# Optimization experiments

Hardware: AMD Instinct MI355X
Metric: run time of the kernel (lower is better)

## Reference

```python
import jax, jax.numpy as jnp
import numpy as np
from math import sqrt

B = 128        # graphs
P = 256        # nodes per graph
N = B * P      # total nodes
E = 524288     # edges (avg degree 16)
S = 32         # seed queries per graph
DQ = DK = DV = 128
H = 4          # heads


def setup_inputs() -> dict:
    key = jax.random.key(0)
    ks = jax.random.split(key, 10)
    Q = jax.random.normal(ks[0], (B, S, DQ), dtype=jnp.float32)
    x = jax.random.normal(ks[1], (N, DK), dtype=jnp.float32)
    # edges constrained within each graph block of P nodes
    src = jax.random.randint(ks[2], (E,), 0, N)
    dst = (src // P) * P + jax.random.randint(ks[3], (E,), 0, P)
    edge_index = jnp.stack([src, dst]).astype(jnp.int64)
    batch = (jnp.arange(N) // P).astype(jnp.int64)
    s = 1.0 / sqrt(DV)
    Wq = jax.random.normal(ks[4], (DQ, DV), dtype=jnp.float32) * s
    Wk = jax.random.normal(ks[5], (DK, DV), dtype=jnp.float32) * s
    Wv = jax.random.normal(ks[6], (DK, DV), dtype=jnp.float32) * s
    Wo = jax.random.normal(ks[7], (DV, DV), dtype=jnp.float32) * s
    z = jnp.zeros((DV,), jnp.float32)
    o = jnp.ones((DV,), jnp.float32)
    return {"Q": Q, "x": x, "edge_index": edge_index, "batch": batch,
            "Wq": Wq, "bq": z, "Wk": Wk, "bk": z, "Wv": Wv, "bv": z,
            "Wo": Wo, "bo": z, "g0": o, "b0": z, "g1": o, "b1": z}


def _gcn(x, edge_index, W, b):
    # PyG GCNConv: self-loops + symmetric deg^-1/2 normalization, then scatter-add
    xw = x @ W                                   # [N, DV]
    row, col = edge_index[0], edge_index[1]
    deg = jnp.zeros((N,), xw.dtype).at[col].add(1.0) + 1.0  # +1 for self-loop
    dinv = jax.lax.rsqrt(deg)
    coef = dinv[row] * dinv[col]                 # [E]
    out = jnp.zeros_like(xw).at[col].add(xw[row] * coef[:, None])
    out = out + xw * (dinv * dinv)[:, None]      # self-loop messages
    return out + b


def _ln(x, g, b, eps=1e-5):
    mu = x.mean(-1, keepdims=True)
    var = ((x - mu) ** 2).mean(-1, keepdims=True)
    return (x - mu) * jax.lax.rsqrt(var + eps) * g + b


def reference(Q, x, edge_index, batch, Wq, bq, Wk, bk, Wv, bv, Wo, bo, g0, b0, g1, b1):
    dh = DV // H
    Qp = Q @ Wq + bq                             # [B, S, DV]
    K = _gcn(x, edge_index, Wk, bk)              # [N, DV]
    V = _gcn(x, edge_index, Wv, bv)
    # to_dense_batch: equal-size graphs -> static reshape; mask all valid
    Kd = K.reshape(B, P, DV)
    Vd = V.reshape(B, P, DV)
    mask = jnp.ones((B, P), Qp.dtype)
    mask_add = (1.0 - mask) * -1e9               # [B, P]
    # split heads on last dim (== torch split(dim=2) + cat(dim=0))
    Qh = Qp.reshape(B, S, H, dh)
    Kh = Kd.reshape(B, P, H, dh)
    Vh = Vd.reshape(B, P, H, dh)
    scores = jnp.einsum('bshd,bphd->bhsp', Qh, Kh) / sqrt(DV)
    A = jax.nn.softmax(scores + mask_add[:, None, None, :], axis=-1)
    Oh = Qh + jnp.einsum('bhsp,bphd->bshd', A, Vh)
    O = Oh.reshape(B, S, DV)
    O = _ln(O, g0, b0)
    O = O + jax.nn.relu(O @ Wo + bo)
    O = _ln(O, g1, b1)
    return O
```

## Files before the change

### kernel.cpp

```cpp
#include <hip/hip_runtime.h>

typedef unsigned int uint32;
typedef unsigned short ushort;
typedef __attribute__((ext_vector_type(8))) short short8;
typedef __attribute__((ext_vector_type(4))) float f32x4;

#define NNODES 32768
#define NGRAPH 128
#define PNODES 256
#define SQ 32
#define NEDGE 524288
#define DIM 128
#define NHEAD 4
#define MAXDEG 64

__device__ __forceinline__ float u2f(uint32 u){ union{uint32 i; float f;} c; c.i=u; return c.f; }
__device__ __forceinline__ uint32 f2bf(float f){
  union{float f; uint32 i;} c; c.f=f;
  return (c.i + 0x7FFFu + ((c.i>>16)&1u)) >> 16;
}
__device__ __forceinline__ uint32 pk2(float a, float b){ return f2bf(a) | (f2bf(b)<<16); }

__global__ __launch_bounds__(256) void k_prep0(const float* __restrict__ Wk,
    const float* __restrict__ Wv, const float* __restrict__ Wq, const float* __restrict__ Wo,
    ushort* __restrict__ WTk, ushort* __restrict__ WTv, ushort* __restrict__ WTq,
    ushort* __restrict__ WTo, int4* __restrict__ zbase){
  const int bid = blockIdx.x;
  const int t = threadIdx.x;
  if (bid >= 4){
    int idx = (bid-4)*256 + t;
    if (idx < 8192) zbase[idx] = int4{0,0,0,0};
    return;
  }
  __shared__ __align__(16) float Ws2[128*132];
  const float* W = (bid==0) ? Wk : (bid==1) ? Wv : (bid==2) ? Wq : Wo;
  ushort* WT     = (bid==0) ? WTk : (bid==1) ? WTv : (bid==2) ? WTq : WTo;
  for (int idx = t; idx < 4096; idx += 256){
    int k = idx >> 5, c4 = idx & 31;
    *(float4*)&Ws2[k*132 + c4*4] = *(const float4*)&W[k*128 + c4*4];
  }
  __syncthreads();
  for (int idx = t; idx < 2048; idx += 256){
    int n = idx & 127, c8 = idx >> 7;
    uint4 p;
    p.x = pk2(Ws2[(c8*8+0)*132 + n], Ws2[(c8*8+1)*132 + n]);
    p.y = pk2(Ws2[(c8*8+2)*132 + n], Ws2[(c8*8+3)*132 + n]);
    p.z = pk2(Ws2[(c8*8+4)*132 + n], Ws2[(c8*8+5)*132 + n]);
    p.w = pk2(Ws2[(c8*8+6)*132 + n], Ws2[(c8*8+7)*132 + n]);
    *(uint4*)&WT[n*128 + c8*8] = p;
  }
}

__global__ void k_edges(const int* __restrict__ ei, int* __restrict__ deg,
                        ushort* __restrict__ ebuf){
  int e = blockIdx.x*256 + threadIdx.x;
  int s = ei[e];
  int d = ei[NEDGE + e];
  int i = atomicAdd(&deg[d], 1);
  if (i < MAXDEG) ebuf[(d << 6) + i] = (ushort)(s & 255);
}

#define APITCH 132
__global__ __launch_bounds__(512) void k_aggkv(
    const int* __restrict__ deg, const ushort* __restrict__ ebuf,
    const float* __restrict__ x,
    const ushort* __restrict__ WTk, const float* __restrict__ bk, ushort* __restrict__ Kb,
    const ushort* __restrict__ WTv, const float* __restrict__ bv, ushort* __restrict__ Vb)
{
  __shared__ __align__(16) char lds[138240];
  uint32* A    = (uint32*)lds;
  ushort* Au   = (ushort*)lds;
  ushort* xT   = (ushort*)(lds + 67584);
  ushort* xa_s = (ushort*)(lds + 67584);
  ushort* wtA  = (ushort*)(lds + 102400);
  ushort* wtB  = (ushort*)(lds + 0);
  ushort* KK   = (ushort*)(lds + 67584);
  ushort* VV   = (ushort*)(lds + 102400);
  float*  dvs  = (float*)(lds + 137216);
  const int t = threadIdx.x;
  const int g = blockIdx.x >> 1, half = blockIdx.x & 1;
  const int base = g*PNODES;
  const int rbase = half*128;

  if (t < 256) dvs[t] = rsqrtf((float)(deg[base + t] + 1));
  {
    uint4* Az = (uint4*)A;
    for (int i = t; i < 4224; i += 512) Az[i] = uint4{0,0,0,0};
  }
  __syncthreads();
  if (t < 128){
    float dn = dvs[rbase + t];
    int src = rbase + t;
    uint32 nb = f2bf(dn*dn);
    A[t*APITCH + (src>>1)] = (src & 1) ? (nb<<16) : nb;
  }
  for (int idx = t; idx < 8192; idx += 512){
    int f = idx & 127, s4 = idx >> 7;
    const int r = base + s4*4;
    float v0 = x[(r+0)*DIM + f];
    float v1 = x[(r+1)*DIM + f];
    float v2 = x[(r+2)*DIM + f];
    float v3 = x[(r+3)*DIM + f];
    uint2 p; p.x = pk2(v0, v1); p.y = pk2(v2, v3);
    *(uint2*)&xT[f*264 + s4*4] = p;
  }
  __syncthreads();
  {
    const int r = t >> 2, sub = t & 3;
    const int n = base + rbase + r;
    const int dg = min(deg[n], MAXDEG);
    const float dn = dvs[rbase + r];
    const ushort* eb = ebuf + (n << 6);
    for (int i = sub; i < dg; i += 4){
      const int srcl = eb[i];
      const float coef = dn * dvs[srcl];
      uint32* cell = &A[r*APITCH + (srcl>>1)];
      const bool hi = srcl & 1;
      uint32 old = *cell, assumed;
      do {
        assumed = old;
        uint32 hb = hi ? (old >> 16) : (old & 0xffffu);
        float cur = u2f(hb << 16);
        uint32 nb = f2bf(cur + coef);
        uint32 nw = hi ? ((old & 0xffffu) | (nb<<16)) : ((old & 0xffff0000u) | nb);
        old = atomicCAS(cell, assumed, nw);
      } while (old != assumed);
    }
  }
  __syncthreads();
  const int lane = t & 63, w = t >> 6;
  const int r16 = lane & 15, kg = lane >> 4;
  f32x4 acc[8];
  #pragma unroll
  for (int j = 0; j < 8; ++j) acc[j] = (f32x4){0.f,0.f,0.f,0.f};
  #pragma unroll
  for (int kc = 0; kc < 8; ++kc){
    const short8 a = *(const short8*)&Au[(w*16 + r16)*264 + kc*32 + kg*8];
    #pragma unroll
    for (int ct = 0; ct < 8; ++ct){
      const short8 b = *(const short8*)&xT[(ct*16 + r16)*264 + kc*32 + kg*8];
      acc[ct] = __builtin_amdgcn_mfma_f32_16x16x32_bf16(a, b, acc[ct], 0, 0, 0);
    }
  }
  __syncthreads();
  #pragma unroll
  for (int ct = 0; ct < 8; ++ct)
    #pragma unroll
    for (int q = 0; q < 4; ++q)
      xa_s[(w*16 + kg*4 + q)*136 + ct*16 + r16] = (ushort)f2bf(acc[ct][q]);
  for (int idx = t; idx < 2048; idx += 512){
    int n = idx >> 4, c8 = idx & 15;
    *(uint4*)&wtA[n*136 + c8*8] = *(const uint4*)&WTk[n*128 + c8*8];
    *(uint4*)&wtB[n*136 + c8*8] = *(const uint4*)&WTv[n*128 + c8*8];
  }
  __syncthreads();
  f32x4 k0[8], v0[8];
  #pragma unroll
  for (int j = 0; j < 8; ++j){ k0[j] = (f32x4){0.f,0.f,0.f,0.f}; v0[j] = (f32x4){0.f,0.f,0.f,0.f}; }
  #pragma unroll
  for (int kc = 0; kc < 4; ++kc){
    const short8 a = *(const short8*)&xa_s[(w*16 + r16)*136 + kc*32 + kg*8];
    #pragma unroll
    for (int ct = 0; ct < 8; ++ct){
      const short8 b0 = *(const short8*)&wtA[(ct*16 + r16)*136 + kc*32 + kg*8];
      const short8 b1 = *(const short8*)&wtB[(ct*16 + r16)*136 + kc*32 + kg*8];
      k0[ct] = __builtin_amdgcn_mfma_f32_16x16x32_bf16(a, b0, k0[ct], 0, 0, 0);
      v0[ct] = __builtin_amdgcn_mfma_f32_16x16x32_bf16(a, b1, v0[ct], 0, 0, 0);
    }
  }
  __syncthreads();
  #pragma unroll
  for (int ct = 0; ct < 8; ++ct){
    const int col = ct*16 + r16;
    const float bkc = bk[col], bvc = bv[col];
    #pragma unroll
    for (int q = 0; q < 4; ++q){
      const int r = w*16 + kg*4 + q;
      KK[r*136 + col] = (ushort)f2bf(k0[ct][q] + bkc);
      VV[r*136 + col] = (ushort)f2bf(v0[ct][q] + bvc);
    }
  }
  __syncthreads();
  for (int idx = t; idx < 2048; idx += 512){
    int r = idx >> 4, c8 = idx & 15;
    *(uint4*)&Kb[(base + rbase + r)*DIM + c8*8] = *(const uint4*)&KK[r*136 + c8*8];
    *(uint4*)&Vb[(base + rbase + r)*DIM + c8*8] = *(const uint4*)&VV[r*136 + c8*8];
  }
}

__global__ __launch_bounds__(512) void k_attnepi(
    const float* __restrict__ Qin, const ushort* __restrict__ WTq,
    const float* __restrict__ bq,
    const ushort* __restrict__ Kb, const ushort* __restrict__ Vb,
    const ushort* __restrict__ WoT, const float* __restrict__ bo,
    const float* __restrict__ g0, const float* __restrict__ b0,
    const float* __restrict__ g1, const float* __restrict__ b1,
    float* __restrict__ out)
{
  __shared__ __align__(16) char lds[151040];
  ushort* KbS = (ushort*)lds;
  ushort* VT  = (ushort*)lds;
  ushort* R2  = (ushort*)(lds + 69632);
  float*  S   = (float*)(lds + 104448);
  float*  Zf  = (float*)(lds + 104448);
  ushort* Pb  = (ushort*)(lds + 121344);
  float*  Yf  = (float*)(lds + 121344);
  float*  Ob  = (float*)(lds + 129792);
  float*  Qres= (float*)(lds + 138240);
  ushort* Qb  = (ushort*)(lds + 146688);

  const int t = threadIdx.x;
  const int w = t >> 6, lane = t & 63;
  const int r16 = lane & 15, kg = lane >> 4;
  const int g = blockIdx.x >> 1, qh = blockIdx.x & 1;
  const int qr0 = g*SQ + qh*16;

  for (int idx = t; idx < 4096; idx += 512){
    int r = idx >> 4, c8 = idx & 15;
    *(uint4*)&KbS[r*136 + c8*8] = *(const uint4*)&Kb[(g*256 + r)*128 + c8*8];
  }
  for (int idx = t; idx < 2048; idx += 512){
    int n = idx >> 4, c8 = idx & 15;
    *(uint4*)&R2[n*136 + c8*8] = *(const uint4*)&WTq[n*128 + c8*8];
  }
  short8 qin[4];
  #pragma unroll
  for (int kc = 0; kc < 4; ++kc){
    const float4 f0 = *(const float4*)&Qin[(qr0 + r16)*128 + kc*32 + kg*8];
    const float4 f1 = *(const float4*)&Qin[(qr0 + r16)*128 + kc*32 + kg*8 + 4];
    union { short8 s; uint32 u[4]; } c;
    c.u[0] = pk2(f0.x, f0.y); c.u[1] = pk2(f0.z, f0.w);
    c.u[2] = pk2(f1.x, f1.y); c.u[3] = pk2(f1.z, f1.w);
    qin[kc] = c.s;
  }
  __syncthreads();

  {
    f32x4 qa = (f32x4){0.f,0.f,0.f,0.f};
    #pragma unroll
    for (int kc = 0; kc < 4; ++kc){
      const short8 bf = *(const short8*)&R2[(w*16 + r16)*136 + kc*32 + kg*8];
      qa = __builtin_amdgcn_mfma_f32_16x16x32_bf16(qin[kc], bf, qa, 0, 0, 0);
    }
    #pragma unroll
    for (int q = 0; q < 4; ++q){
      const int row = kg*4 + q, col = w*16 + r16;
      const float v = qa[q] + bq[col];
      Qres[row*132 + col] = v;
      Qb[row*136 + col] = (ushort)f2bf(v);
    }
  }
  __syncthreads();

  {
    short8 qf[4];
    #pragma unroll
    for (int kc = 0; kc < 4; ++kc)
      qf[kc] = *(const short8*)&Qb[r16*136 + kc*32 + kg*8];
    f32x4 sa[2];
    sa[0] = (f32x4){0.f,0.f,0.f,0.f}; sa[1] = (f32x4){0.f,0.f,0.f,0.f};
    #pragma unroll
    for (int kc = 0; kc < 4; ++kc){
      #pragma unroll
      for (int nt = 0; nt < 2; ++nt){
        const short8 bf = *(const short8*)&KbS[((w*2+nt)*16 + r16)*136 + kc*32 + kg*8];
        sa[nt] = __builtin_amdgcn_mfma_f32_16x16x32_bf16(qf[kc], bf, sa[nt], 0, 0, 0);
      }
    }
    #pragma unroll
    for (int nt = 0; nt < 2; ++nt)
      #pragma unroll
      for (int q = 0; q < 4; ++q)
        S[(kg*4+q)*264 + (w*2+nt)*16 + r16] = sa[nt][q] * 0.08838834764831845f;
  }
  __syncthreads();

  {
    const int row = t >> 5, j = t & 31;
    float vals[8];
    float m = -1e30f;
    #pragma unroll
    for (int u = 0; u < 8; ++u){
      vals[u] = S[row*264 + j + 32*u];
      m = fmaxf(m, vals[u]);
    }
    m = fmaxf(m, __shfl_xor(m, 1));
    m = fmaxf(m, __shfl_xor(m, 2));
    m = fmaxf(m, __shfl_xor(m, 4));
    m = fmaxf(m, __shfl_xor(m, 8));
    m = fmaxf(m, __shfl_xor(m, 16));
    float sum = 0.f;
    #pragma unroll
    for (int u = 0; u < 8; ++u){
      vals[u] = __expf(vals[u] - m);
      sum += vals[u];
    }
    sum += __shfl_xor(sum, 1);
    sum += __shfl_xor(sum, 2);
    sum += __shfl_xor(sum, 4);
    sum += __shfl_xor(sum, 8);
    sum += __shfl_xor(sum, 16);
    float inv = 1.f / sum;
    #pragma unroll
    for (int u = 0; u < 8; ++u)
      Pb[row*264 + j + 32*u] = (ushort)f2bf(vals[u] * inv);
  }
  for (int idx = t; idx < 4096; idx += 512){
    int p = idx & 255, c8 = idx >> 8;
    uint4 v = *(const uint4*)&Vb[(g*256 + p)*128 + c8*8];
    const ushort* u = (const ushort*)&v;
    #pragma unroll
    for (int j2 = 0; j2 < 8; ++j2)
      VT[(c8*8 + j2)*264 + p] = u[j2];
  }
  __syncthreads();

  {
    f32x4 oa = (f32x4){0.f,0.f,0.f,0.f};
    #pragma unroll
    for (int kc = 0; kc < 8; ++kc){
      const short8 pa = *(const short8*)&Pb[r16*264 + kc*32 + kg*8];
      const short8 vb = *(const short8*)&VT[(w*16 + r16)*264 + kc*32 + kg*8];
      oa = __builtin_amdgcn_mfma_f32_16x16x32_bf16(pa, vb, oa, 0, 0, 0);
    }
    #pragma unroll
    for (int q = 0; q < 4; ++q){
      const int row = kg*4 + q, col = w*16 + r16;
      Ob[row*132 + col] = oa[q] + Qres[row*132 + col];
    }
  }
  __syncthreads();

  #pragma unroll
  for (int rr = 0; rr < 2; ++rr){
    const int row = w*2 + rr;
    float x0 = Ob[row*132 + 2*lane], x1 = Ob[row*132 + 2*lane + 1];
    float s = x0 + x1;
    s += __shfl_xor(s,1); s += __shfl_xor(s,2); s += __shfl_xor(s,4);
    s += __shfl_xor(s,8); s += __shfl_xor(s,16); s += __shfl_xor(s,32);
    float mu = s * 0.0078125f;
    float d0 = x0 - mu, d1 = x1 - mu;
    float vv = d0*d0 + d1*d1;
    vv += __shfl_xor(vv,1); vv += __shfl_xor(vv,2); vv += __shfl_xor(vv,4);
    vv += __shfl_xor(vv,8); vv += __shfl_xor(vv,16); vv += __shfl_xor(vv,32);
    float rs = rsqrtf(vv*0.0078125f + 1e-5f);
    const float2 gv = *(const float2*)&g0[2*lane];
    const float2 bv = *(const float2*)&b0[2*lane];
    float y0 = d0*rs*gv.x + bv.x;
    float y1 = d1*rs*gv.y + bv.y;
    Yf[row*132 + 2*lane] = y0; Yf[row*132 + 2*lane + 1] = y1;
    *(uint32*)&Qb[row*136 + 2*lane] = pk2(y0, y1);
  }
  for (int idx = t; idx < 2048; idx += 512){
    int n = idx >> 4, c8 = idx & 15;
    *(uint4*)&R2[n*136 + c8*8] = *(const uint4*)&WoT[n*128 + c8*8];
  }
  __syncthreads();

  {
    f32x4 fa = (f32x4){0.f,0.f,0.f,0.f};
    #pragma unroll
    for (int kc = 0; kc < 4; ++kc){
      const short8 ya = *(const short8*)&Qb[r16*136 + kc*32 + kg*8];
      const short8 wb = *(const short8*)&R2[(w*16 + r16)*136 + kc*32 + kg*8];
      fa = __builtin_amdgcn_mfma_f32_16x16x32_bf16(ya, wb, fa, 0, 0, 0);
    }
    #pragma unroll
    for (int q = 0; q < 4; ++q){
      const int row = kg*4 + q, col = w*16 + r16;
      Zf[row*132 + col] = Yf[row*132 + col] + fmaxf(fa[q] + bo[col], 0.f);
    }
  }
  __syncthreads();

  #pragma unroll
  for (int rr = 0; rr < 2; ++rr){
    const int row = w*2 + rr;
    float z0 = Zf[row*132 + 2*lane], z1 = Zf[row*132 + 2*lane + 1];
    float s = z0 + z1;
    s += __shfl_xor(s,1); s += __shfl_xor(s,2); s += __shfl_xor(s,4);
    s += __shfl_xor(s,8); s += __shfl_xor(s,16); s += __shfl_xor(s,32);
    float mu = s * 0.0078125f;
    float d0 = z0 - mu, d1 = z1 - mu;
    float vv = d0*d0 + d1*d1;
    vv += __shfl_xor(vv,1); vv += __shfl_xor(vv,2); vv += __shfl_xor(vv,4);
    vv += __shfl_xor(vv,8); vv += __shfl_xor(vv,16); vv += __shfl_xor(vv,32);
    float rs = rsqrtf(vv*0.0078125f + 1e-5f);
    const float2 g1v = *(const float2*)&g1[2*lane];
    const float2 b1v = *(const float2*)&b1[2*lane];
    float2 o;
    o.x = d0*rs*g1v.x + b1v.x;
    o.y = d1*rs*g1v.y + b1v.y;
    *(float2*)&out[(qr0 + row)*128 + 2*lane] = o;
  }
}

extern "C" void kernel_launch(void* const* d_in, const int* in_sizes, int n_in,
                              void* d_out, int out_size, void* d_ws, size_t ws_size,
                              hipStream_t stream){
  const float* Q   = (const float*)d_in[0];
  const float* x   = (const float*)d_in[1];
  const int*   ei  = (const int*)d_in[2];
  const float* Wq  = (const float*)d_in[4];
  const float* bq  = (const float*)d_in[5];
  const float* Wk  = (const float*)d_in[6];
  const float* bk  = (const float*)d_in[7];
  const float* Wv  = (const float*)d_in[8];
  const float* bv  = (const float*)d_in[9];
  const float* Wo  = (const float*)d_in[10];
  const float* bo  = (const float*)d_in[11];
  const float* g0  = (const float*)d_in[12];
  const float* b0  = (const float*)d_in[13];
  const float* g1  = (const float*)d_in[14];
  const float* b1  = (const float*)d_in[15];

  char* ws = (char*)d_ws;
  ushort* Kb   = (ushort*)(ws);
  ushort* Vb   = (ushort*)(ws + 8388608);
  ushort* WTk  = (ushort*)(ws + 16777216);
  ushort* WTv  = (ushort*)(ws + 16809984);
  ushort* WTq  = (ushort*)(ws + 16842752);
  ushort* WTo  = (ushort*)(ws + 16875520);
  int*    deg  = (int*)(ws + 16908288);
  ushort* ebuf = (ushort*)(ws + 17039360);

  k_prep0<<<36, 256, 0, stream>>>(Wk, Wv, Wq, Wo, WTk, WTv, WTq, WTo, (int4*)deg);
  k_edges<<<NEDGE/256, 256, 0, stream>>>(ei, deg, ebuf);
  k_aggkv<<<NGRAPH*2, 512, 0, stream>>>(deg, ebuf, x, WTk, bk, Kb, WTv, bv, Vb);
  k_attnepi<<<NGRAPH*2, 512, 0, stream>>>(Q, WTq, bq, Kb, Vb, WTo, bo, g0, b0, g1, b1, (float*)d_out);
}
```

Baseline: 73.81 us.

## Store V transposed, read K/V/weights directly from global in attention, split queries finer

The aggregation kernel now writes V in a transposed per-graph layout, so the attention kernel can feed MFMA B operands straight from global memory instead of staging K, V and the weight matrices in LDS. The attention kernel shrinks to 256 threads with a small LDS footprint and 4 blocks per graph (8 query rows each), which raises occupancy and parallelism. The edge accumulation replaces its CAS loop with plain read-modify-writes, with each sub-lane owning the word pairs whose index mod 4 matches it. In exchange, half the MFMA rows are padding, K and V are re-read from global or L2 by four blocks per graph, and some loads are uncoalesced. Every sub-lane now scans the full edge list.

```diff
diff --git a/kernel.cpp b/kernel.cpp
--- a/kernel.cpp
+++ b/kernel.cpp
@@ -65,7 +65,7 @@
     const int* __restrict__ deg, const ushort* __restrict__ ebuf,
     const float* __restrict__ x,
     const ushort* __restrict__ WTk, const float* __restrict__ bk, ushort* __restrict__ Kb,
-    const ushort* __restrict__ WTv, const float* __restrict__ bv, ushort* __restrict__ Vb)
+    const ushort* __restrict__ WTv, const float* __restrict__ bv, ushort* __restrict__ VbT)
 {
   __shared__ __align__(16) char lds[138240];
   uint32* A    = (uint32*)lds;
@@ -75,7 +75,7 @@
   ushort* wtA  = (ushort*)(lds + 102400);
   ushort* wtB  = (ushort*)(lds + 0);
   ushort* KK   = (ushort*)(lds + 67584);
-  ushort* VV   = (ushort*)(lds + 102400);
+  ushort* VVt  = (ushort*)(lds + 102400);
   float*  dvs  = (float*)(lds + 137216);
   const int t = threadIdx.x;
   const int g = blockIdx.x >> 1, half = blockIdx.x & 1;
@@ -111,20 +111,19 @@
     const int dg = min(deg[n], MAXDEG);
     const float dn = dvs[rbase + r];
     const ushort* eb = ebuf + (n << 6);
-    for (int i = sub; i < dg; i += 4){
+    for (int i = 0; i < dg; ++i){
       const int srcl = eb[i];
+      if (((srcl >> 1) & 3) != sub) continue;
       const float coef = dn * dvs[srcl];
       uint32* cell = &A[r*APITCH + (srcl>>1)];
-      const bool hi = srcl & 1;
-      uint32 old = *cell, assumed;
-      do {
-        assumed = old;
-        uint32 hb = hi ? (old >> 16) : (old & 0xffffu);
-        float cur = u2f(hb << 16);
-        uint32 nb = f2bf(cur + coef);
-        uint32 nw = hi ? ((old & 0xffffu) | (nb<<16)) : ((old & 0xffff0000u) | nb);
-        old = atomicCAS(cell, assumed, nw);
-      } while (old != assumed);
+      uint32 old = *cell;
+      if (srcl & 1){
+        float cur = u2f(old & 0xffff0000u);
+        *cell = (old & 0xffffu) | (f2bf(cur + coef) << 16);
+      } else {
+        float cur = u2f(old << 16);
+        *cell = (old & 0xffff0000u) | f2bf(cur + coef);
+      }
     }
   }
   __syncthreads();
@@ -176,78 +175,86 @@
     #pragma unroll
     for (int q = 0; q < 4; ++q){
       const int r = w*16 + kg*4 + q;
-      KK[r*136 + col] = (ushort)f2bf(k0[ct][q] + bkc);
-      VV[r*136 + col] = (ushort)f2bf(v0[ct][q] + bvc);
+      KK[r*136 + col]  = (ushort)f2bf(k0[ct][q] + bkc);
+      VVt[col*136 + r] = (ushort)f2bf(v0[ct][q] + bvc);
     }
   }
   __syncthreads();
   for (int idx = t; idx < 2048; idx += 512){
     int r = idx >> 4, c8 = idx & 15;
     *(uint4*)&Kb[(base + rbase + r)*DIM + c8*8] = *(const uint4*)&KK[r*136 + c8*8];
-    *(uint4*)&Vb[(base + rbase + r)*DIM + c8*8] = *(const uint4*)&VV[r*136 + c8*8];
-  }
-}
-
-__global__ __launch_bounds__(512) void k_attnepi(
+  }
+  for (int idx = t; idx < 2048; idx += 512){
+    int d = idx >> 4, c8 = idx & 15;
+    *(uint4*)&VbT[(g*128 + d)*PNODES + rbase + c8*8] = *(const uint4*)&VVt[d*136 + c8*8];
+  }
+}
+
+__global__ __launch_bounds__(256) void k_attnepi(
     const float* __restrict__ Qin, const ushort* __restrict__ WTq,
     const float* __restrict__ bq,
-    const ushort* __restrict__ Kb, const ushort* __restrict__ Vb,
+    const ushort* __restrict__ Kb, const ushort* __restrict__ VbT,
     const ushort* __restrict__ WoT, const float* __restrict__ bo,
     const float* __restrict__ g0, const float* __restrict__ b0,
     const float* __restrict__ g1, const float* __restrict__ b1,
     float* __restrict__ out)
 {
-  __shared__ __align__(16) char lds[151040];
-  ushort* KbS = (ushort*)lds;
-  ushort* VT  = (ushort*)lds;
-  ushort* R2  = (ushort*)(lds + 69632);
-  float*  S   = (float*)(lds + 104448);
-  float*  Zf  = (float*)(lds + 104448);
-  ushort* Pb  = (ushort*)(lds + 121344);
-  float*  Yf  = (float*)(lds + 121344);
-  float*  Ob  = (float*)(lds + 129792);
-  float*  Qres= (float*)(lds + 138240);
-  ushort* Qb  = (ushort*)(lds + 146688);
+  __shared__ __align__(16) char lds[29696];
+  ushort* Qb  = (ushort*)lds;
+  ushort* Pb  = (ushort*)(lds + 4352);
+  float*  S   = (float*)(lds + 12800);
+  float*  Qres= (float*)(lds + 21248);
+  float*  Ob  = (float*)(lds + 25472);
+  float*  Yf  = (float*)(lds + 4352);
+  float*  Zf  = (float*)(lds + 12800);
 
   const int t = threadIdx.x;
   const int w = t >> 6, lane = t & 63;
   const int r16 = lane & 15, kg = lane >> 4;
-  const int g = blockIdx.x >> 1, qh = blockIdx.x & 1;
-  const int qr0 = g*SQ + qh*16;
-
-  for (int idx = t; idx < 4096; idx += 512){
-    int r = idx >> 4, c8 = idx & 15;
-    *(uint4*)&KbS[r*136 + c8*8] = *(const uint4*)&Kb[(g*256 + r)*128 + c8*8];
-  }
-  for (int idx = t; idx < 2048; idx += 512){
-    int n = idx >> 4, c8 = idx & 15;
-    *(uint4*)&R2[n*136 + c8*8] = *(const uint4*)&WTq[n*128 + c8*8];
-  }
-  short8 qin[4];
-  #pragma unroll
-  for (int kc = 0; kc < 4; ++kc){
-    const float4 f0 = *(const float4*)&Qin[(qr0 + r16)*128 + kc*32 + kg*8];
-    const float4 f1 = *(const float4*)&Qin[(qr0 + r16)*128 + kc*32 + kg*8 + 4];
-    union { short8 s; uint32 u[4]; } c;
-    c.u[0] = pk2(f0.x, f0.y); c.u[1] = pk2(f0.z, f0.w);
-    c.u[2] = pk2(f1.x, f1.y); c.u[3] = pk2(f1.z, f1.w);
-    qin[kc] = c.s;
-  }
-  __syncthreads();
-
-  {
-    f32x4 qa = (f32x4){0.f,0.f,0.f,0.f};
-    #pragma unroll
-    for (int kc = 0; kc < 4; ++kc){
-      const short8 bf = *(const short8*)&R2[(w*16 + r16)*136 + kc*32 + kg*8];
-      qa = __builtin_amdgcn_mfma_f32_16x16x32_bf16(qin[kc], bf, qa, 0, 0, 0);
-    }
-    #pragma unroll
-    for (int q = 0; q < 4; ++q){
-      const int row = kg*4 + q, col = w*16 + r16;
-      const float v = qa[q] + bq[col];
-      Qres[row*132 + col] = v;
-      Qb[row*136 + col] = (ushort)f2bf(v);
+  const int g = blockIdx.x >> 2, qq = blockIdx.x & 3;
+  const int qr0 = g*SQ + qq*8;
+
+  {
+    uint4* z1 = (uint4*)lds;
+    for (int i = t; i < 800; i += 256) z1[i] = uint4{0,0,0,0};
+  }
+  __syncthreads();
+
+  {
+    short8 qa_[4];
+    if (r16 < 8){
+      #pragma unroll
+      for (int kc = 0; kc < 4; ++kc){
+        const float4 f0 = *(const float4*)&Qin[(qr0 + r16)*128 + kc*32 + kg*8];
+        const float4 f1 = *(const float4*)&Qin[(qr0 + r16)*128 + kc*32 + kg*8 + 4];
+        union { short8 s; uint32 u[4]; } c;
+        c.u[0] = pk2(f0.x,f0.y); c.u[1] = pk2(f0.z,f0.w);
+        c.u[2] = pk2(f1.x,f1.y); c.u[3] = pk2(f1.z,f1.w);
+        qa_[kc] = c.s;
+      }
+    } else {
+      #pragma unroll
+      for (int kc = 0; kc < 4; ++kc) qa_[kc] = (short8){0,0,0,0,0,0,0,0};
+    }
+    #pragma unroll
+    for (int j = 0; j < 2; ++j){
+      const int ct = w*2 + j;
+      f32x4 qa = (f32x4){0.f,0.f,0.f,0.f};
+      #pragma unroll
+      for (int kc = 0; kc < 4; ++kc){
+        const short8 bf = *(const short8*)&WTq[(ct*16 + r16)*128 + kc*32 + kg*8];
+        qa = __builtin_amdgcn_mfma_f32_16x16x32_bf16(qa_[kc], bf, qa, 0, 0, 0);
+      }
+      #pragma unroll
+      for (int q = 0; q < 4; ++q){
+        const int row = kg*4 + q;
+        if (row < 8){
+          const int col = ct*16 + r16;
+          const float v = qa[q] + bq[col];
+          Qres[row*132 + col] = v;
+          Qb[row*136 + col] = (ushort)f2bf(v);
+        }
+      }
     }
   }
   __syncthreads();
@@ -257,21 +264,22 @@
     #pragma unroll
     for (int kc = 0; kc < 4; ++kc)
       qf[kc] = *(const short8*)&Qb[r16*136 + kc*32 + kg*8];
-    f32x4 sa[2];
-    sa[0] = (f32x4){0.f,0.f,0.f,0.f}; sa[1] = (f32x4){0.f,0.f,0.f,0.f};
-    #pragma unroll
-    for (int kc = 0; kc < 4; ++kc){
-      #pragma unroll
-      for (int nt = 0; nt < 2; ++nt){
-        const short8 bf = *(const short8*)&KbS[((w*2+nt)*16 + r16)*136 + kc*32 + kg*8];
-        sa[nt] = __builtin_amdgcn_mfma_f32_16x16x32_bf16(qf[kc], bf, sa[nt], 0, 0, 0);
-      }
-    }
-    #pragma unroll
-    for (int nt = 0; nt < 2; ++nt)
-      #pragma unroll
-      for (int q = 0; q < 4; ++q)
-        S[(kg*4+q)*264 + (w*2+nt)*16 + r16] = sa[nt][q] * 0.08838834764831845f;
+    #pragma unroll
+    for (int nt = 0; nt < 4; ++nt){
+      const int kt = w*4 + nt;
+      f32x4 sa = (f32x4){0.f,0.f,0.f,0.f};
+      #pragma unroll
+      for (int kc = 0; kc < 4; ++kc){
+        const short8 bf = *(const short8*)&Kb[(g*256 + kt*16 + r16)*128 + kc*32 + kg*8];
+        sa = __builtin_amdgcn_mfma_f32_16x16x32_bf16(qf[kc], bf, sa, 0, 0, 0);
+      }
+      #pragma unroll
+      for (int q = 0; q < 4; ++q){
+        const int row = kg*4 + q;
+        if (row < 8)
+          S[row*264 + kt*16 + r16] = sa[q] * 0.08838834764831845f;
+      }
+    }
   }
   __syncthreads();
 
@@ -305,28 +313,30 @@
     for (int u = 0; u < 8; ++u)
       Pb[row*264 + j + 32*u] = (ushort)f2bf(vals[u] * inv);
   }
-  for (int idx = t; idx < 4096; idx += 512){
-    int p = idx & 255, c8 = idx >> 8;
-    uint4 v = *(const uint4*)&Vb[(g*256 + p)*128 + c8*8];
-    const ushort* u = (const ushort*)&v;
-    #pragma unroll
-    for (int j2 = 0; j2 < 8; ++j2)
-      VT[(c8*8 + j2)*264 + p] = u[j2];
-  }
-  __syncthreads();
-
-  {
-    f32x4 oa = (f32x4){0.f,0.f,0.f,0.f};
-    #pragma unroll
-    for (int kc = 0; kc < 8; ++kc){
-      const short8 pa = *(const short8*)&Pb[r16*264 + kc*32 + kg*8];
-      const short8 vb = *(const short8*)&VT[(w*16 + r16)*264 + kc*32 + kg*8];
-      oa = __builtin_amdgcn_mfma_f32_16x16x32_bf16(pa, vb, oa, 0, 0, 0);
-    }
-    #pragma unroll
-    for (int q = 0; q < 4; ++q){
-      const int row = kg*4 + q, col = w*16 + r16;
-      Ob[row*132 + col] = oa[q] + Qres[row*132 + col];
+  __syncthreads();
+
+  {
+    short8 pa[8];
+    #pragma unroll
+    for (int kc = 0; kc < 8; ++kc)
+      pa[kc] = *(const short8*)&Pb[r16*264 + kc*32 + kg*8];
+    #pragma unroll
+    for (int j = 0; j < 2; ++j){
+      const int dt = w*2 + j;
+      f32x4 oa = (f32x4){0.f,0.f,0.f,0.f};
+      #pragma unroll
+      for (int kc = 0; kc < 8; ++kc){
+        const short8 vb = *(const short8*)&VbT[(g*128 + dt*16 + r16)*PNODES + kc*32 + kg*8];
+        oa = __builtin_amdgcn_mfma_f32_16x16x32_bf16(pa[kc], vb, oa, 0, 0, 0);
+      }
+      #pragma unroll
+      for (int q = 0; q < 4; ++q){
+        const int row = kg*4 + q;
+        if (row < 8){
+          const int col = dt*16 + r16;
+          Ob[row*132 + col] = oa[q] + Qres[row*132 + col];
+        }
+      }
     }
   }
   __syncthreads();
@@ -351,24 +361,30 @@
     Yf[row*132 + 2*lane] = y0; Yf[row*132 + 2*lane + 1] = y1;
     *(uint32*)&Qb[row*136 + 2*lane] = pk2(y0, y1);
   }
-  for (int idx = t; idx < 2048; idx += 512){
-    int n = idx >> 4, c8 = idx & 15;
-    *(uint4*)&R2[n*136 + c8*8] = *(const uint4*)&WoT[n*128 + c8*8];
-  }
-  __syncthreads();
-
-  {
-    f32x4 fa = (f32x4){0.f,0.f,0.f,0.f};
-    #pragma unroll
-    for (int kc = 0; kc < 4; ++kc){
-      const short8 ya = *(const short8*)&Qb[r16*136 + kc*32 + kg*8];
-      const short8 wb = *(const short8*)&R2[(w*16 + r16)*136 + kc*32 + kg*8];
-      fa = __builtin_amdgcn_mfma_f32_16x16x32_bf16(ya, wb, fa, 0, 0, 0);
-    }
-    #pragma unroll
-    for (int q = 0; q < 4; ++q){
-      const int row = kg*4 + q, col = w*16 + r16;
-      Zf[row*132 + col] = Yf[row*132 + col] + fmaxf(fa[q] + bo[col], 0.f);
+  __syncthreads();
+
+  {
+    short8 ya[4];
+    #pragma unroll
+    for (int kc = 0; kc < 4; ++kc)
+      ya[kc] = *(const short8*)&Qb[r16*136 + kc*32 + kg*8];
+    #pragma unroll
+    for (int j = 0; j < 2; ++j){
+      const int ct = w*2 + j;
+      f32x4 fa = (f32x4){0.f,0.f,0.f,0.f};
+      #pragma unroll
+      for (int kc = 0; kc < 4; ++kc){
+        const short8 wb = *(const short8*)&WoT[(ct*16 + r16)*128 + kc*32 + kg*8];
+        fa = __builtin_amdgcn_mfma_f32_16x16x32_bf16(ya[kc], wb, fa, 0, 0, 0);
+      }
+      #pragma unroll
+      for (int q = 0; q < 4; ++q){
+        const int row = kg*4 + q;
+        if (row < 8){
+          const int col = ct*16 + r16;
+          Zf[row*132 + col] = Yf[row*132 + col] + fmaxf(fa[q] + bo[col], 0.f);
+        }
+      }
     }
   }
   __syncthreads();
@@ -416,7 +432,7 @@
 
   char* ws = (char*)d_ws;
   ushort* Kb   = (ushort*)(ws);
-  ushort* Vb   = (ushort*)(ws + 8388608);
+  ushort* VbT  = (ushort*)(ws + 8388608);
   ushort* WTk  = (ushort*)(ws + 16777216);
   ushort* WTv  = (ushort*)(ws + 16809984);
   ushort* WTq  = (ushort*)(ws + 16842752);
@@ -426,6 +442,6 @@
 
   k_prep0<<<36, 256, 0, stream>>>(Wk, Wv, Wq, Wo, WTk, WTv, WTq, WTo, (int4*)deg);
   k_edges<<<NEDGE/256, 256, 0, stream>>>(ei, deg, ebuf);
-  k_aggkv<<<NGRAPH*2, 512, 0, stream>>>(deg, ebuf, x, WTk, bk, Kb, WTv, bv, Vb);
-  k_attnepi<<<NGRAPH*2, 512, 0, stream>>>(Q, WTq, bq, Kb, Vb, WTo, bo, g0, b0, g1, b1, (float*)d_out);
-}
+  k_aggkv<<<NGRAPH*2, 512, 0, stream>>>(deg, ebuf, x, WTk, bk, Kb, WTv, bv, VbT);
+  k_attnepi<<<NGRAPH*4, 256, 0, stream>>>(Q, WTq, bq, Kb, VbT, WTo, bo, g0, b0, g1, b1, (float*)d_out);
+}
```

Result: slower. 80.85 us (+9.5%).

## Store V transposed in global memory and partition edge scatter to drop CAS loops

Applied to the files above, without the earlier changes.

The V projection is now written to global memory in a per-graph transposed layout [dim][node], so the attention kernel loads V^T with straight 16-byte copies instead of element-wise transposing through LDS. In the adjacency build, each of the 4 threads per row owns the LDS cells whose index mod 4 equals its lane, so updates become plain read-modify-write with no atomicCAS retry loop. In exchange, every thread now scans the full edge list for its row, and the transposed writes in the aggregation kernel are 2-byte scattered LDS stores.

```diff
diff --git a/kernel.cpp b/kernel.cpp
--- a/kernel.cpp
+++ b/kernel.cpp
@@ -65,7 +65,7 @@
     const int* __restrict__ deg, const ushort* __restrict__ ebuf,
     const float* __restrict__ x,
     const ushort* __restrict__ WTk, const float* __restrict__ bk, ushort* __restrict__ Kb,
-    const ushort* __restrict__ WTv, const float* __restrict__ bv, ushort* __restrict__ Vb)
+    const ushort* __restrict__ WTv, const float* __restrict__ bv, ushort* __restrict__ VbT)
 {
   __shared__ __align__(16) char lds[138240];
   uint32* A    = (uint32*)lds;
@@ -75,7 +75,7 @@
   ushort* wtA  = (ushort*)(lds + 102400);
   ushort* wtB  = (ushort*)(lds + 0);
   ushort* KK   = (ushort*)(lds + 67584);
-  ushort* VV   = (ushort*)(lds + 102400);
+  ushort* VVt  = (ushort*)(lds + 102400);
   float*  dvs  = (float*)(lds + 137216);
   const int t = threadIdx.x;
   const int g = blockIdx.x >> 1, half = blockIdx.x & 1;
@@ -111,20 +111,19 @@
     const int dg = min(deg[n], MAXDEG);
     const float dn = dvs[rbase + r];
     const ushort* eb = ebuf + (n << 6);
-    for (int i = sub; i < dg; i += 4){
+    for (int i = 0; i < dg; ++i){
       const int srcl = eb[i];
+      if (((srcl >> 1) & 3) != sub) continue;
       const float coef = dn * dvs[srcl];
       uint32* cell = &A[r*APITCH + (srcl>>1)];
-      const bool hi = srcl & 1;
-      uint32 old = *cell, assumed;
-      do {
-        assumed = old;
-        uint32 hb = hi ? (old >> 16) : (old & 0xffffu);
-        float cur = u2f(hb << 16);
-        uint32 nb = f2bf(cur + coef);
-        uint32 nw = hi ? ((old & 0xffffu) | (nb<<16)) : ((old & 0xffff0000u) | nb);
-        old = atomicCAS(cell, assumed, nw);
-      } while (old != assumed);
+      uint32 old = *cell;
+      if (srcl & 1){
+        float cur = u2f(old & 0xffff0000u);
+        *cell = (old & 0xffffu) | (f2bf(cur + coef) << 16);
+      } else {
+        float cur = u2f(old << 16);
+        *cell = (old & 0xffff0000u) | f2bf(cur + coef);
+      }
     }
   }
   __syncthreads();
@@ -176,22 +175,25 @@
     #pragma unroll
     for (int q = 0; q < 4; ++q){
       const int r = w*16 + kg*4 + q;
-      KK[r*136 + col] = (ushort)f2bf(k0[ct][q] + bkc);
-      VV[r*136 + col] = (ushort)f2bf(v0[ct][q] + bvc);
+      KK[r*136 + col]  = (ushort)f2bf(k0[ct][q] + bkc);
+      VVt[col*136 + r] = (ushort)f2bf(v0[ct][q] + bvc);
     }
   }
   __syncthreads();
   for (int idx = t; idx < 2048; idx += 512){
     int r = idx >> 4, c8 = idx & 15;
     *(uint4*)&Kb[(base + rbase + r)*DIM + c8*8] = *(const uint4*)&KK[r*136 + c8*8];
-    *(uint4*)&Vb[(base + rbase + r)*DIM + c8*8] = *(const uint4*)&VV[r*136 + c8*8];
+  }
+  for (int idx = t; idx < 2048; idx += 512){
+    int d = idx >> 4, c8 = idx & 15;
+    *(uint4*)&VbT[(g*128 + d)*PNODES + rbase + c8*8] = *(const uint4*)&VVt[d*136 + c8*8];
   }
 }
 
 __global__ __launch_bounds__(512) void k_attnepi(
     const float* __restrict__ Qin, const ushort* __restrict__ WTq,
     const float* __restrict__ bq,
-    const ushort* __restrict__ Kb, const ushort* __restrict__ Vb,
+    const ushort* __restrict__ Kb, const ushort* __restrict__ VbT,
     const ushort* __restrict__ WoT, const float* __restrict__ bo,
     const float* __restrict__ g0, const float* __restrict__ b0,
     const float* __restrict__ g1, const float* __restrict__ b1,
@@ -306,12 +308,8 @@
       Pb[row*264 + j + 32*u] = (ushort)f2bf(vals[u] * inv);
   }
   for (int idx = t; idx < 4096; idx += 512){
-    int p = idx & 255, c8 = idx >> 8;
-    uint4 v = *(const uint4*)&Vb[(g*256 + p)*128 + c8*8];
-    const ushort* u = (const ushort*)&v;
-    #pragma unroll
-    for (int j2 = 0; j2 < 8; ++j2)
-      VT[(c8*8 + j2)*264 + p] = u[j2];
+    int d = idx >> 5, c8 = idx & 31;
+    *(uint4*)&VT[d*264 + c8*8] = *(const uint4*)&VbT[(g*128 + d)*PNODES + c8*8];
   }
   __syncthreads();
 
@@ -416,7 +414,7 @@
 
   char* ws = (char*)d_ws;
   ushort* Kb   = (ushort*)(ws);
-  ushort* Vb   = (ushort*)(ws + 8388608);
+  ushort* VbT  = (ushort*)(ws + 8388608);
   ushort* WTk  = (ushort*)(ws + 16777216);
   ushort* WTv  = (ushort*)(ws + 16809984);
   ushort* WTq  = (ushort*)(ws + 16842752);
@@ -426,6 +424,6 @@
 
   k_prep0<<<36, 256, 0, stream>>>(Wk, Wv, Wq, Wo, WTk, WTv, WTq, WTo, (int4*)deg);
   k_edges<<<NEDGE/256, 256, 0, stream>>>(ei, deg, ebuf);
-  k_aggkv<<<NGRAPH*2, 512, 0, stream>>>(deg, ebuf, x, WTk, bk, Kb, WTv, bv, Vb);
-  k_attnepi<<<NGRAPH*2, 512, 0, stream>>>(Q, WTq, bq, Kb, Vb, WTo, bo, g0, b0, g1, b1, (float*)d_out);
-}
+  k_aggkv<<<NGRAPH*2, 512, 0, stream>>>(deg, ebuf, x, WTk, bk, Kb, WTv, bv, VbT);
+  k_attnepi<<<NGRAPH*2, 512, 0, stream>>>(Q, WTq, bq, Kb, VbT, WTo, bo, g0, b0, g1, b1, (float*)d_out);
+}
```

Measured after the change: 73.78 us. Within noise of the previous version (-0.0%).
